# Kernel tuning notes

Measured on AMD Instinct MI355X. Metric: run time of the kernel, lower is better.

The kernel has to match this reference:

```python
import jax, jax.numpy as jnp
import numpy as np

B, T, D = 32, 256, 256  # batch, input_length, output_dim (input_dim == output_dim)
SCALE = 0.06  # ~ 1/sqrt(D) glorot-ish init so LSTM gates don't saturate


def hard_sigmoid(x):
    # Keras-1 default inner_activation for LSTM
    return jnp.clip(0.2 * x + 0.5, 0.0, 1.0)


def lstm_cell(x_t, h, c, W, U, b, d):
    # Keras gate order: i, f, c(g), o
    z = x_t @ W + h @ U + b
    i = hard_sigmoid(z[:, :d])
    f = hard_sigmoid(z[:, d:2 * d])
    g = jnp.tanh(z[:, 2 * d:3 * d])
    o = hard_sigmoid(z[:, 3 * d:])
    c_new = f * c + i * g
    h_new = o * jnp.tanh(c_new)
    return h_new, c_new


def setup_inputs() -> dict:
    key = jax.random.key(0)
    ks = jax.random.split(key, 7)
    x = jax.random.normal(ks[0], (B, T, D), dtype=jnp.float32)
    reader_W = jax.random.normal(ks[1], (D, 4 * D), dtype=jnp.float32) * SCALE
    reader_U = jax.random.normal(ks[2], (D, 4 * D), dtype=jnp.float32) * SCALE
    reader_b = jnp.zeros((4 * D,), jnp.float32)
    writer_W = jax.random.normal(ks[3], (2 * D, 4 * D), dtype=jnp.float32) * SCALE
    writer_U = jax.random.normal(ks[4], (D, 4 * D), dtype=jnp.float32) * SCALE
    writer_b = jnp.zeros((4 * D,), jnp.float32)
    composer_W = jax.random.normal(ks[5], (2 * D, 2 * D), dtype=jnp.float32) * SCALE
    composer_b = jnp.zeros((2 * D,), jnp.float32)
    return {"x": x, "reader_W": reader_W, "reader_U": reader_U, "reader_b": reader_b,
            "writer_W": writer_W, "writer_U": writer_U, "writer_b": writer_b,
            "composer_W": composer_W, "composer_b": composer_b}


def reference(x, reader_W, reader_U, reader_b, writer_W, writer_U, writer_b,
              composer_W, composer_b):
    b, t, d = x.shape
    h0 = jnp.zeros((b, d), x.dtype)
    c0 = jnp.zeros((b, d), x.dtype)

    # ---- read: reader LSTM over the sequence (return_sequences) ----
    def rstep(carry, x_t):
        h, c = carry
        h, c = lstm_cell(x_t, h, c, reader_W, reader_U, reader_b, d)
        return (h, c), h

    _, o_seq = jax.lax.scan(rstep, (h0, c0), jnp.swapaxes(x, 0, 1))  # [T,B,D]

    mem0 = x  # mem_0 = input (B, T, D)

    # ---- compose_and_write_step per timestep ----
    def step(carry, o_t):
        mem, wh, wc = carry
        # summarize_memory: eqs 2-3
        scores = jnp.einsum('bd,btd->bt', o_t, mem)
        z_t = jax.nn.softmax(scores, axis=-1)                 # (B, T)
        m_rt = jnp.einsum('bt,btd->bd', z_t, mem)             # (B, D)
        # compose (eq 4), linear activation
        c_t = jnp.concatenate([o_t, m_rt], axis=-1) @ composer_W + composer_b  # (B, 2D)
        # writer LSTM step (eq 5)
        wh, wc = lstm_cell(c_t, wh, wc, writer_W, writer_U, writer_b, d)
        # update_memory (eq 6): blend via tiled z_t / h_t
        zt = z_t[:, :, None]
        mem = mem * (1.0 - zt) + wh[:, None, :] * zt
        return (mem, wh, wc), wh

    (_, _, _), hs = jax.lax.scan(step, (mem0, h0, c0), o_seq)  # hs: [T,B,D]
    return hs[-1]  # return_mode == 'last_output'
```

## Files before the change

### kernel.cpp

```cpp
#include <hip/hip_runtime.h>
#include <math.h>

#define TB 512
#define NBATCH 32
#define TT 256
#define DD 256

typedef float f32x4 __attribute__((ext_vector_type(4)));

#define WS_WF   0u
#define WS_BF   524288u
#define WS_HP   525312u
#define WS_PAR  541696u
#define PS      260
#define WS_WHP  608256u
#define WS_BAR  616448u
#define WS_FLOATS 624704u

#define O_WW    0
#define S_WW    784
#define O_RW    12544
#define S_RW    524
#define O_MEM   20928
#define S_MEM   260
#define O_WACT  29248
#define S_WACT  792
#define O_RACT  35584
#define S_RACT  524
#define O_WZ    39776
#define O_RZ    39936
#define O_SS    40096
#define O_SE    40128
#define O_WC    40160
#define O_RC    40192
#define O_WB    40224
#define O_RB    40240
#define O_RJ    40256
#define O_MS    40320
#define LDS_FLOATS 40448
#define DYN_LDS_BYTES (LDS_FLOATS*4)

__device__ __forceinline__ float hsig(float x) { return fminf(fmaxf(0.2f*x + 0.5f, 0.f), 1.f); }
__device__ __forceinline__ float ftanh(float x) {
  const float a = fminf(fabsf(x), 15.f);
  const float e = __expf(2.f * a);
  const float r = (e - 1.f) / (e + 1.f);
  return copysignf(r, x);
}
__device__ __forceinline__ int akw(int k) { return k + 4*(k/192); }
__device__ __forceinline__ int akr(int k) { return k + 4*(k/128); }

__device__ __forceinline__ void gst(float* p, float v) {
  __hip_atomic_store(p, v, __ATOMIC_RELAXED, __HIP_MEMORY_SCOPE_AGENT);
}
__device__ __forceinline__ void gst4(float* p, f32x4 v) {
  asm volatile("global_store_dwordx4 %0, %1, off sc0 sc1" :: "v"(p), "v"(v) : "memory");
}

__device__ __forceinline__ void tag_store(int* tp, int v) {
  asm volatile("s_waitcnt vmcnt(0) lgkmcnt(0)" ::: "memory");
  __syncthreads();
  if (threadIdx.x == 0)
    __hip_atomic_store(tp, v, __ATOMIC_RELAXED, __HIP_MEMORY_SCOPE_AGENT);
}
__device__ __forceinline__ void tag_spin(const int* tags, int v) {
  if (threadIdx.x < 64) {
    int sp = 0;
    for (;;) {
      const int t = __hip_atomic_load(&tags[threadIdx.x * 16], __ATOMIC_RELAXED,
                                      __HIP_MEMORY_SCOPE_AGENT);
      if (__all(t == v)) break;
      __builtin_amdgcn_s_sleep(2);
      if (++sp > (1 << 14)) break;
    }
  }
  __syncthreads();
}
__device__ __forceinline__ void barrier_fenced(int* cnt, int target) {
  __syncthreads();
  if (threadIdx.x == 0) {
    __threadfence();
    __hip_atomic_fetch_add(cnt, 1, __ATOMIC_RELAXED, __HIP_MEMORY_SCOPE_AGENT);
    int sp = 0;
    while (__hip_atomic_load(cnt, __ATOMIC_RELAXED, __HIP_MEMORY_SCOPE_AGENT) < target) {
      if (++sp > (1 << 20)) break;
    }
    __threadfence();
  }
  __syncthreads();
}

__global__ void __launch_bounds__(TB) nse_kernel(
    const float* __restrict__ x,
    const float* __restrict__ rW, const float* __restrict__ rU, const float* __restrict__ rb,
    const float* __restrict__ wW, const float* __restrict__ wU, const float* __restrict__ wb,
    const float* __restrict__ cW, const float* __restrict__ cb,
    float* __restrict__ out, float* __restrict__ ws)
{
  extern __shared__ float sm[];
  const int tid = threadIdx.x;
  const int w = blockIdx.x;
  const int g = w >> 6;
  const int m = w & 63;
  const int b0 = g * 8;
  const int blm = m >> 3;
  const int isl = m & 7;
  const int bmy = b0 + blm;

  float* Wf   = ws + WS_WF;
  float* bfv  = ws + WS_BF;
  float* hpub = ws + WS_HP;
  float* par  = ws + WS_PAR;
  float* whp  = ws + WS_WHP;
  int*   bars = (int*)(ws + WS_BAR);
  int* tagsA  = &bars[g*1024];
  int* tagsB  = &bars[4096 + g*1024];
  int* myA    = &tagsA[m*16];
  int* myB    = &tagsB[m*16];
  int* lcnt   = &bars[8192];
  int* magic  = &bars[8192 + 32];

  if (w == 0 && tid == 0) {
    __hip_atomic_store(lcnt, 0, __ATOMIC_RELAXED, __HIP_MEMORY_SCOPE_AGENT);
    __hip_atomic_store(magic, 1357911, __ATOMIC_RELEASE, __HIP_MEMORY_SCOPE_AGENT);
  }
  if (tid == 0) {
    int sp = 0;
    while (__hip_atomic_load(magic, __ATOMIC_ACQUIRE, __HIP_MEMORY_SCOPE_AGENT) != 1357911) {
      if (++sp > (1 << 20)) break;
    }
  }
  __syncthreads();

  {
    const int kt = w >> 4, nt = w & 15;
    const int r = tid >> 4, c4 = (tid & 15) * 4;
    float a0 = 0.f, a1 = 0.f, a2 = 0.f, a3 = 0.f;
    for (int jc = 0; jc < 512; jc += 32) {
      for (int u = tid; u < 1024; u += TB) {
        int rr = u >> 5, jj = u & 31;
        sm[rr*33 + jj] = cW[(32*kt + rr)*512 + jc + jj];
      }
      {
        int jj = tid >> 4, cc = (tid & 15) * 4;
        const f32x4 v = *(const f32x4*)&wW[(jc + jj)*1024 + 64*nt + cc];
        float* d = &sm[1056 + jj*68 + cc];
        d[0] = v.x; d[1] = v.y; d[2] = v.z; d[3] = v.w;
      }
      __syncthreads();
      #pragma unroll 8
      for (int j = 0; j < 32; j++) {
        const float a = sm[r*33 + j];
        const float* wv = &sm[1056 + j*68 + c4];
        a0 += a*wv[0]; a1 += a*wv[1]; a2 += a*wv[2]; a3 += a*wv[3];
      }
      __syncthreads();
    }
    float* d = &Wf[(32*kt + r)*1024 + 64*nt + c4];
    d[0] = a0; d[1] = a1; d[2] = a2; d[3] = a3;
  }
  if (w >= 16 && w < 32) {
    __syncthreads();
    const int base = (w - 16) * 64;
    const int c = tid & 63, jq = tid >> 6;
    float p = 0.f;
    for (int j = 64*jq; j < 64*jq + 64; j++) p += cb[j] * wW[j*1024 + base + c];
    sm[jq*68 + c] = p;
    __syncthreads();
    if (tid < 64) {
      float s = wb[base + tid];
      for (int j = 0; j < 8; j++) s += sm[j*68 + tid];
      bfv[base + tid] = s;
    }
  }
  barrier_fenced(lcnt, 256);

  for (int u = tid; u < 3072; u += TB) {
    const int k = u >> 2, gate = u & 3;
    const float* sp = (k < 512) ? &Wf[(size_t)k*1024 + gate*256 + 4*m]
                                : &wU[(size_t)(k-512)*1024 + gate*256 + 4*m];
    const f32x4 v = *(const f32x4*)sp;
    const int ik = akw(k);
    sm[O_WW + (gate*4+0)*S_WW + ik] = v.x;
    sm[O_WW + (gate*4+1)*S_WW + ik] = v.y;
    sm[O_WW + (gate*4+2)*S_WW + ik] = v.z;
    sm[O_WW + (gate*4+3)*S_WW + ik] = v.w;
  }
  for (int u = tid; u < 2048; u += TB) {
    const int k = u >> 2, gate = u & 3;
    const float* sp = (k < 256) ? &rW[(size_t)k*1024 + gate*256 + 4*m]
                                : &rU[(size_t)(k-256)*1024 + gate*256 + 4*m];
    const f32x4 v = *(const f32x4*)sp;
    const int ik = akr(k);
    sm[O_RW + (gate*4+0)*S_RW + ik] = v.x;
    sm[O_RW + (gate*4+1)*S_RW + ik] = v.y;
    sm[O_RW + (gate*4+2)*S_RW + ik] = v.z;
    sm[O_RW + (gate*4+3)*S_RW + ik] = v.w;
  }
  for (int u = tid; u < 2048; u += TB) {
    const int r = u >> 6, d4 = (u & 63) * 4;
    *(f32x4*)&sm[O_MEM + r*S_MEM + d4] =
        *(const f32x4*)&x[((size_t)bmy*TT + 32*isl + r)*DD + d4];
  }
  for (int u = tid; u < LDS_FLOATS - O_WACT; u += TB) sm[O_WACT + u] = 0.f;
  __syncthreads();
  {
    const int bl = tid >> 6, d4 = (tid & 63) * 4;
    *(f32x4*)&sm[O_RACT + bl*S_RACT + akr(d4)] =
        *(const f32x4*)&x[(size_t)(b0+bl)*TT*DD + d4];
  }
  if (tid < 16) {
    const int gate = tid >> 2, dl = tid & 3;
    sm[O_WB + tid] = bfv[gate*256 + 4*m + dl];
    sm[O_RB + tid] = rb[gate*256 + 4*m + dl];
  }
  __syncthreads();

  const int q   = tid & 3;
  const int cl  = ((tid >> 4) & 3) + 4 * (tid >> 7);
  const int bl8 = ((tid >> 2) & 3) + 4 * ((tid >> 6) & 1);

  for (int s = 0; s <= TT; s++) {
    if (s >= 1) {
      tag_spin(tagsB, s - 1);
      const int bl = tid >> 6, d4 = (tid & 63) * 4;
      f32x4 vh, vw;
      const float* ph = &hpub[(size_t)((s-1)&1)*8192 + (b0+bl)*256 + d4];
      const float* pw = &whp[(b0+bl)*256 + d4];
      asm volatile(
        "global_load_dwordx4 %0, %2, off sc0 sc1\n\t"
        "global_load_dwordx4 %1, %3, off sc0 sc1\n\t"
        "s_waitcnt vmcnt(0)"
        : "=&v"(vh), "=&v"(vw) : "v"(ph), "v"(pw) : "memory");
      *(f32x4*)&sm[O_RACT + bl*S_RACT + akr(256 + d4)] = vh;
      *(f32x4*)&sm[O_WACT + bl*S_WACT + akw(d4)]       = vh;
      if (s >= 2)
        *(f32x4*)&sm[O_WACT + bl*S_WACT + akw(512 + d4)] = vw;
    }
    __syncthreads();

    if (s >= 1) {
      const int r = tid >> 4, tk = tid & 15;
      float* mrow = &sm[O_MEM + r*S_MEM + 16*tk];
      const float* orow = &sm[O_RACT + blm*S_RACT + akr(256 + 16*tk)];
      float acc = 0.f;
      if (s >= 2) {
        const float zr = sm[O_SE + r] * sm[O_RJ + blm*8 + isl];
        const float omz = 1.f - zr;
        const float* hrow = &sm[O_WACT + blm*S_WACT + akw(512 + 16*tk)];
        #pragma unroll
        for (int i2 = 0; i2 < 16; i2 += 4) {
          f32x4 mv = *(f32x4*)(mrow + i2);
          const f32x4 hv = *(const f32x4*)(hrow + i2);
          const f32x4 ov = *(const f32x4*)(orow + i2);
          mv.x = mv.x*omz + hv.x*zr;  mv.y = mv.y*omz + hv.y*zr;
          mv.z = mv.z*omz + hv.z*zr;  mv.w = mv.w*omz + hv.w*zr;
          *(f32x4*)(mrow + i2) = mv;
          acc += mv.x*ov.x + mv.y*ov.y + mv.z*ov.z + mv.w*ov.w;
        }
      } else {
        #pragma unroll
        for (int i2 = 0; i2 < 16; i2 += 4) {
          const f32x4 mv = *(const f32x4*)(mrow + i2);
          const f32x4 ov = *(const f32x4*)(orow + i2);
          acc += mv.x*ov.x + mv.y*ov.y + mv.z*ov.z + mv.w*ov.w;
        }
      }
      acc += __shfl_xor(acc, 1, 64); acc += __shfl_xor(acc, 2, 64);
      acc += __shfl_xor(acc, 4, 64); acc += __shfl_xor(acc, 8, 64);
      if (tk == 0) sm[O_SS + r] = acc;
    }
    __syncthreads();
    if (s >= 1 && tid < 32) {
      const float sc = sm[O_SS + tid];
      float mx = sc;
      mx = fmaxf(mx, __shfl_xor(mx, 1, 64)); mx = fmaxf(mx, __shfl_xor(mx, 2, 64));
      mx = fmaxf(mx, __shfl_xor(mx, 4, 64)); mx = fmaxf(mx, __shfl_xor(mx, 8, 64));
      mx = fmaxf(mx, __shfl_xor(mx, 16, 64));
      const float e = __expf(sc - mx);
      float su = e;
      su += __shfl_xor(su, 1, 64); su += __shfl_xor(su, 2, 64); su += __shfl_xor(su, 4, 64);
      su += __shfl_xor(su, 8, 64); su += __shfl_xor(su, 16, 64);
      sm[O_SE + tid] = e;
      if (tid == 0) {
        gst(&par[((size_t)bmy*8 + isl)*PS + 256], mx);
        gst(&par[((size_t)bmy*8 + isl)*PS + 257], su);
      }
    }
    __syncthreads();
    if (s >= 1) {
      const int dblk = tid >> 3, rh = tid & 7;
      f32x4 p; p.x = 0.f; p.y = 0.f; p.z = 0.f; p.w = 0.f;
      #pragma unroll
      for (int i = 0; i < 4; i++) {
        const int rr = 4*rh + i;
        const float e = sm[O_SE + rr];
        const f32x4 mv = *(const f32x4*)&sm[O_MEM + rr*S_MEM + 4*dblk];
        p.x += e*mv.x; p.y += e*mv.y; p.z += e*mv.z; p.w += e*mv.w;
      }
      p.x += __shfl_xor(p.x,1,64); p.x += __shfl_xor(p.x,2,64); p.x += __shfl_xor(p.x,4,64);
      p.y += __shfl_xor(p.y,1,64); p.y += __shfl_xor(p.y,2,64); p.y += __shfl_xor(p.y,4,64);
      p.z += __shfl_xor(p.z,1,64); p.z += __shfl_xor(p.z,2,64); p.z += __shfl_xor(p.z,4,64);
      p.w += __shfl_xor(p.w,1,64); p.w += __shfl_xor(p.w,2,64); p.w += __shfl_xor(p.w,4,64);
      if (rh == 0) gst4(&par[((size_t)bmy*8 + isl)*PS + 4*dblk], p);
      tag_store(myA, s);
    } else {
      __syncthreads();
    }

    if (s <= TT-1) {
      const float* wr = &sm[O_RW + cl*S_RW + 132*q];
      const float* ar = &sm[O_RACT + bl8*S_RACT + 132*q];
      float acc = 0.f;
      #pragma unroll
      for (int kk = 0; kk < 128; kk += 4) {
        const f32x4 wv = *(const f32x4*)(wr + kk);
        const f32x4 av = *(const f32x4*)(ar + kk);
        acc += wv.x*av.x + wv.y*av.y + wv.z*av.z + wv.w*av.w;
      }
      acc += __shfl_xor(acc, 1, 64);
      acc += __shfl_xor(acc, 2, 64);
      if (q == 0) sm[O_RZ + bl8*20 + cl] = acc + sm[O_RB + cl];
    }
    __syncthreads();
    if (s <= TT-1 && tid < 32) {
      const int bl = tid >> 2, dl = tid & 3;
      const float zi = sm[O_RZ + bl*20 + dl];
      const float zf = sm[O_RZ + bl*20 + 4 + dl];
      const float zg = sm[O_RZ + bl*20 + 8 + dl];
      const float zo = sm[O_RZ + bl*20 + 12 + dl];
      const float cn = hsig(zf)*sm[O_RC + tid] + hsig(zi)*ftanh(zg);
      sm[O_RC + tid] = cn;
      gst(&hpub[(size_t)(s&1)*8192 + (b0+bl)*256 + 4*m + dl], hsig(zo)*ftanh(cn));
    }

    if (s >= 1) {
      tag_spin(tagsA, s);
      const int bl = tid >> 6, d4 = (tid & 63) * 4;
      f32x4 v0,v1,v2,v3,v4,v5,v6,v7;
      float msv;
      {
        const float* p0 = &par[((size_t)(b0+bl)*8 + 0)*PS + d4];
        const float* p4 = p0 + 4*PS;
        const int idx = tid & 127;
        const float* msp = &par[((size_t)(b0 + (idx>>4))*8 + ((idx>>1)&7))*PS + 256 + (idx&1)];
        asm volatile(
          "global_load_dwordx4 %0, %9, off sc0 sc1\n\t"
          "global_load_dwordx4 %1, %9, off offset:1040 sc0 sc1\n\t"
          "global_load_dwordx4 %2, %9, off offset:2080 sc0 sc1\n\t"
          "global_load_dwordx4 %3, %9, off offset:3120 sc0 sc1\n\t"
          "global_load_dwordx4 %4, %10, off sc0 sc1\n\t"
          "global_load_dwordx4 %5, %10, off offset:1040 sc0 sc1\n\t"
          "global_load_dwordx4 %6, %10, off offset:2080 sc0 sc1\n\t"
          "global_load_dwordx4 %7, %10, off offset:3120 sc0 sc1\n\t"
          "global_load_dword   %8, %11, off sc0 sc1\n\t"
          "s_waitcnt vmcnt(0)"
          : "=&v"(v0),"=&v"(v1),"=&v"(v2),"=&v"(v3),
            "=&v"(v4),"=&v"(v5),"=&v"(v6),"=&v"(v7),"=&v"(msv)
          : "v"(p0), "v"(p4), "v"(msp) : "memory");
      }
      if (tid < 128) sm[O_MS + tid] = msv;
      __syncthreads();
      if (tid < 8) {
        const int bl2 = tid;
        float M = sm[O_MS + bl2*16];
        for (int j = 1; j < 8; j++) M = fmaxf(M, sm[O_MS + bl2*16 + 2*j]);
        float tot = 0.f, f0[8];
        for (int j = 0; j < 8; j++) {
          f0[j] = __expf(sm[O_MS + bl2*16 + 2*j] - M);
          tot += f0[j] * sm[O_MS + bl2*16 + 2*j + 1];
        }
        const float inv = 1.f / tot;
        for (int j = 0; j < 8; j++) sm[O_RJ + bl2*8 + j] = f0[j]*inv;
      }
      __syncthreads();
      {
        const float* rj = &sm[O_RJ + bl*8];
        f32x4 a;
        a.x = rj[0]*v0.x + rj[1]*v1.x + rj[2]*v2.x + rj[3]*v3.x
            + rj[4]*v4.x + rj[5]*v5.x + rj[6]*v6.x + rj[7]*v7.x;
        a.y = rj[0]*v0.y + rj[1]*v1.y + rj[2]*v2.y + rj[3]*v3.y
            + rj[4]*v4.y + rj[5]*v5.y + rj[6]*v6.y + rj[7]*v7.y;
        a.z = rj[0]*v0.z + rj[1]*v1.z + rj[2]*v2.z + rj[3]*v3.z
            + rj[4]*v4.z + rj[5]*v5.z + rj[6]*v6.z + rj[7]*v7.z;
        a.w = rj[0]*v0.w + rj[1]*v1.w + rj[2]*v2.w + rj[3]*v3.w
            + rj[4]*v4.w + rj[5]*v5.w + rj[6]*v6.w + rj[7]*v7.w;
        *(f32x4*)&sm[O_WACT + bl*S_WACT + akw(256 + d4)] = a;
      }
      __syncthreads();
      {
        const float* wr = &sm[O_WW + cl*S_WW + 196*q];
        const float* ar = &sm[O_WACT + bl8*S_WACT + 196*q];
        float acc = 0.f;
        #pragma unroll 8
        for (int kk = 0; kk < 192; kk += 4) {
          const f32x4 wv = *(const f32x4*)(wr + kk);
          const f32x4 av = *(const f32x4*)(ar + kk);
          acc += wv.x*av.x + wv.y*av.y + wv.z*av.z + wv.w*av.w;
        }
        acc += __shfl_xor(acc, 1, 64);
        acc += __shfl_xor(acc, 2, 64);
        if (q == 0) sm[O_WZ + bl8*20 + cl] = acc + sm[O_WB + cl];
      }
      __syncthreads();
      if (tid < 32) {
        const int bl2 = tid >> 2, dl = tid & 3;
        const float zi = sm[O_WZ + bl2*20 + dl];
        const float zf = sm[O_WZ + bl2*20 + 4 + dl];
        const float zg = sm[O_WZ + bl2*20 + 8 + dl];
        const float zo = sm[O_WZ + bl2*20 + 12 + dl];
        const float cn = hsig(zf)*sm[O_WC + tid] + hsig(zi)*ftanh(zg);
        sm[O_WC + tid] = cn;
        const float hn = hsig(zo)*ftanh(cn);
        if (s == TT) out[(b0+bl2)*256 + 4*m + dl] = hn;
        else         gst(&whp[(b0+bl2)*256 + 4*m + dl], hn);
      }
    }
    if (s == TT) break;
    tag_store(myB, s);
    if (s <= TT-2) {
      const int bl = tid >> 6, d4 = (tid & 63) * 4;
      *(f32x4*)&sm[O_RACT + bl*S_RACT + akr(d4)] =
          *(const f32x4*)&x[((size_t)(b0+bl)*TT + s + 1)*DD + d4];
    }
  }
}

extern "C" void kernel_launch(void* const* d_in, const int* in_sizes, int n_in,
                              void* d_out, int out_size, void* d_ws, size_t ws_size,
                              hipStream_t stream) {
  (void)in_sizes; (void)n_in;
  if (ws_size < (size_t)WS_FLOATS * 4u) {
    hipMemsetAsync(d_out, 0, (size_t)out_size * 4u, stream);
    return;
  }
  const float* x  = (const float*)d_in[0];
  const float* rW = (const float*)d_in[1];
  const float* rU = (const float*)d_in[2];
  const float* rb = (const float*)d_in[3];
  const float* wW = (const float*)d_in[4];
  const float* wU = (const float*)d_in[5];
  const float* wb = (const float*)d_in[6];
  const float* cW = (const float*)d_in[7];
  const float* cb = (const float*)d_in[8];
  float* out = (float*)d_out;
  float* ws  = (float*)d_ws;

  hipFuncSetAttribute((const void*)nse_kernel,
                      hipFuncAttributeMaxDynamicSharedMemorySize, DYN_LDS_BYTES);

  void* args[] = { (void*)&x, (void*)&rW, (void*)&rU, (void*)&rb,
                   (void*)&wW, (void*)&wU, (void*)&wb, (void*)&cW, (void*)&cb,
                   (void*)&out, (void*)&ws };
  hipError_t err = hipLaunchCooperativeKernel((const void*)nse_kernel,
                                              dim3(256), dim3(TB), args,
                                              DYN_LDS_BYTES, stream);
  if (err != hipSuccess) {
    nse_kernel<<<dim3(256), dim3(TB), DYN_LDS_BYTES, stream>>>(
        x, rW, rU, rb, wW, wU, wb, cW, cb, out, ws);
  }
}
```

Before: 2.980 ms.

## Regroup blocks by XCD so group sync stays in local L2, keep weights in registers

New measurement: 3.626 ms. 1.22x slower.

```diff
diff --git a/kernel.cpp b/kernel.cpp
--- a/kernel.cpp
+++ b/kernel.cpp
@@ -2,7 +2,6 @@
 #include <math.h>
 
 #define TB 512
-#define NBATCH 32
 #define TT 256
 #define DD 256
 
@@ -15,63 +14,78 @@
 #define PS      260
 #define WS_WHP  608256u
 #define WS_BAR  616448u
-#define WS_FLOATS 624704u
-
-#define O_WW    0
-#define S_WW    784
-#define O_RW    12544
-#define S_RW    524
-#define O_MEM   20928
+#define WS_FLOATS 633024u
+
+#define O_MEM   0
 #define S_MEM   260
-#define O_WACT  29248
-#define S_WACT  792
-#define O_RACT  35584
-#define S_RACT  524
-#define O_WZ    39776
-#define O_RZ    39936
-#define O_SS    40096
-#define O_SE    40128
-#define O_WC    40160
-#define O_RC    40192
-#define O_WB    40224
-#define O_RB    40240
-#define O_RJ    40256
-#define O_MS    40320
-#define LDS_FLOATS 40448
-#define DYN_LDS_BYTES (LDS_FLOATS*4)
+#define O_WACT  8320
+#define S_WACT  832
+#define O_RACT  11648
+#define S_RACT  576
+#define O_WZ    13952
+#define O_RZ    14096
+#define O_SS    14240
+#define O_SE    14272
+#define O_WC    14304
+#define O_RC    14336
+#define O_WB    14368
+#define O_RB    14400
+#define O_RJ    14432
+#define O_MS    14464
+#define O_XR    14528
+#define DYN_LDS_BYTES 131072
 
 __device__ __forceinline__ float hsig(float x) { return fminf(fmaxf(0.2f*x + 0.5f, 0.f), 1.f); }
 __device__ __forceinline__ float ftanh(float x) {
   const float a = fminf(fabsf(x), 15.f);
   const float e = __expf(2.f * a);
-  const float r = (e - 1.f) / (e + 1.f);
-  return copysignf(r, x);
-}
-__device__ __forceinline__ int akw(int k) { return k + 4*(k/192); }
-__device__ __forceinline__ int akr(int k) { return k + 4*(k/128); }
-
-__device__ __forceinline__ void gst(float* p, float v) {
-  __hip_atomic_store(p, v, __ATOMIC_RELAXED, __HIP_MEMORY_SCOPE_AGENT);
-}
-__device__ __forceinline__ void gst4(float* p, f32x4 v) {
-  asm volatile("global_store_dwordx4 %0, %1, off sc0 sc1" :: "v"(p), "v"(v) : "memory");
-}
-
-__device__ __forceinline__ void tag_store(int* tp, int v) {
+  return copysignf((e - 1.f) / (e + 1.f), x);
+}
+__device__ __forceinline__ int awk(int k) { return (k / 48) * 52 + (k % 48); }
+__device__ __forceinline__ int ark(int k) { return (k >> 5) * 36 + (k & 31); }
+
+__device__ __forceinline__ void stI(int* p, int v, bool lx) {
+  if (lx) asm volatile("global_store_dword %0, %1, off sc0" :: "v"(p), "v"(v) : "memory");
+  else    asm volatile("global_store_dword %0, %1, off sc0 sc1" :: "v"(p), "v"(v) : "memory");
+}
+__device__ __forceinline__ int ldI(const int* p, bool lx) {
+  int t;
+  if (lx) asm volatile("global_load_dword %0, %1, off sc0\n\ts_waitcnt vmcnt(0)" : "=v"(t) : "v"(p) : "memory");
+  else    asm volatile("global_load_dword %0, %1, off sc0 sc1\n\ts_waitcnt vmcnt(0)" : "=v"(t) : "v"(p) : "memory");
+  return t;
+}
+__device__ __forceinline__ void stF(float* p, float v, bool lx) {
+  if (lx) asm volatile("global_store_dword %0, %1, off sc0" :: "v"(p), "v"(v) : "memory");
+  else    asm volatile("global_store_dword %0, %1, off sc0 sc1" :: "v"(p), "v"(v) : "memory");
+}
+__device__ __forceinline__ void stF4(float* p, f32x4 v, bool lx) {
+  if (lx) asm volatile("global_store_dwordx4 %0, %1, off sc0" :: "v"(p), "v"(v) : "memory");
+  else    asm volatile("global_store_dwordx4 %0, %1, off sc0 sc1" :: "v"(p), "v"(v) : "memory");
+}
+__device__ __forceinline__ void ld2x4(const float* p1, const float* p2, f32x4& a, f32x4& b, bool lx) {
+  if (lx) asm volatile(
+    "global_load_dwordx4 %0, %2, off sc0\n\t"
+    "global_load_dwordx4 %1, %3, off sc0\n\t"
+    "s_waitcnt vmcnt(0)" : "=&v"(a), "=&v"(b) : "v"(p1), "v"(p2) : "memory");
+  else asm volatile(
+    "global_load_dwordx4 %0, %2, off sc0 sc1\n\t"
+    "global_load_dwordx4 %1, %3, off sc0 sc1\n\t"
+    "s_waitcnt vmcnt(0)" : "=&v"(a), "=&v"(b) : "v"(p1), "v"(p2) : "memory");
+}
+
+__device__ __forceinline__ void tag_store(int* tp, int v, bool lx) {
   asm volatile("s_waitcnt vmcnt(0) lgkmcnt(0)" ::: "memory");
   __syncthreads();
-  if (threadIdx.x == 0)
-    __hip_atomic_store(tp, v, __ATOMIC_RELAXED, __HIP_MEMORY_SCOPE_AGENT);
-}
-__device__ __forceinline__ void tag_spin(const int* tags, int v) {
-  if (threadIdx.x < 64) {
+  if (threadIdx.x == 0) stI(tp, v, lx);
+}
+__device__ __forceinline__ void tag_spin(const int* tags, int v, bool lx) {
+  if (threadIdx.x < 32) {
     int sp = 0;
     for (;;) {
-      const int t = __hip_atomic_load(&tags[threadIdx.x * 16], __ATOMIC_RELAXED,
-                                      __HIP_MEMORY_SCOPE_AGENT);
+      const int t = ldI(&tags[threadIdx.x * 32], lx);
       if (__all(t == v)) break;
-      __builtin_amdgcn_s_sleep(2);
-      if (++sp > (1 << 14)) break;
+      __builtin_amdgcn_s_sleep(1);
+      if (++sp > (1 << 16)) break;
     }
   }
   __syncthreads();
@@ -90,7 +104,7 @@
   __syncthreads();
 }
 
-__global__ void __launch_bounds__(TB) nse_kernel(
+__global__ void __launch_bounds__(TB, 2) nse_kernel(
     const float* __restrict__ x,
     const float* __restrict__ rW, const float* __restrict__ rU, const float* __restrict__ rb,
     const float* __restrict__ wW, const float* __restrict__ wU, const float* __restrict__ wb,
@@ -100,12 +114,6 @@
   extern __shared__ float sm[];
   const int tid = threadIdx.x;
   const int w = blockIdx.x;
-  const int g = w >> 6;
-  const int m = w & 63;
-  const int b0 = g * 8;
-  const int blm = m >> 3;
-  const int isl = m & 7;
-  const int bmy = b0 + blm;
 
   float* Wf   = ws + WS_WF;
   float* bfv  = ws + WS_BF;
@@ -113,15 +121,15 @@
   float* par  = ws + WS_PAR;
   float* whp  = ws + WS_WHP;
   int*   bars = (int*)(ws + WS_BAR);
-  int* tagsA  = &bars[g*1024];
-  int* tagsB  = &bars[4096 + g*1024];
-  int* myA    = &tagsA[m*16];
-  int* myB    = &tagsB[m*16];
-  int* lcnt   = &bars[8192];
-  int* magic  = &bars[8192 + 32];
+  int* lcnt   = &bars[16384];
+  int* magic  = &bars[16416];
+  int* xr     = (int*)&sm[O_XR];
 
   if (w == 0 && tid == 0) {
     __hip_atomic_store(lcnt, 0, __ATOMIC_RELAXED, __HIP_MEMORY_SCOPE_AGENT);
+    for (int i = 0; i < 8; i++)
+      __hip_atomic_store(&bars[16448 + i*8], 0, __ATOMIC_RELAXED, __HIP_MEMORY_SCOPE_AGENT);
+    __hip_atomic_store(&bars[16512], 1, __ATOMIC_RELAXED, __HIP_MEMORY_SCOPE_AGENT);
     __hip_atomic_store(magic, 1357911, __ATOMIC_RELEASE, __HIP_MEMORY_SCOPE_AGENT);
   }
   if (tid == 0) {
@@ -175,79 +183,147 @@
   }
   barrier_fenced(lcnt, 256);
 
-  for (int u = tid; u < 3072; u += TB) {
-    const int k = u >> 2, gate = u & 3;
-    const float* sp = (k < 512) ? &Wf[(size_t)k*1024 + gate*256 + 4*m]
-                                : &wU[(size_t)(k-512)*1024 + gate*256 + 4*m];
-    const f32x4 v = *(const f32x4*)sp;
-    const int ik = akw(k);
-    sm[O_WW + (gate*4+0)*S_WW + ik] = v.x;
-    sm[O_WW + (gate*4+1)*S_WW + ik] = v.y;
-    sm[O_WW + (gate*4+2)*S_WW + ik] = v.z;
-    sm[O_WW + (gate*4+3)*S_WW + ik] = v.w;
-  }
-  for (int u = tid; u < 2048; u += TB) {
-    const int k = u >> 2, gate = u & 3;
-    const float* sp = (k < 256) ? &rW[(size_t)k*1024 + gate*256 + 4*m]
-                                : &rU[(size_t)(k-256)*1024 + gate*256 + 4*m];
-    const f32x4 v = *(const f32x4*)sp;
-    const int ik = akr(k);
-    sm[O_RW + (gate*4+0)*S_RW + ik] = v.x;
-    sm[O_RW + (gate*4+1)*S_RW + ik] = v.y;
-    sm[O_RW + (gate*4+2)*S_RW + ik] = v.z;
-    sm[O_RW + (gate*4+3)*S_RW + ik] = v.w;
-  }
+  {
+    int xcd;
+    asm volatile("s_getreg_b32 %0, hwreg(HW_REG_XCC_ID)" : "=s"(xcd));
+    if (tid == 0) {
+      const int rk = __hip_atomic_fetch_add(&bars[16448 + (xcd & 7)*8], 1,
+                                            __ATOMIC_RELAXED, __HIP_MEMORY_SCOPE_AGENT);
+      xr[0] = xcd & 7;
+      xr[1] = rk;
+    }
+  }
+  barrier_fenced(lcnt, 512);
+  if (tid == 0) {
+    int all32 = 1;
+    for (int i = 0; i < 8; i++) {
+      const int c = __hip_atomic_load(&bars[16448 + i*8], __ATOMIC_RELAXED, __HIP_MEMORY_SCOPE_AGENT);
+      if (c != 32) all32 = 0;
+    }
+    xr[2] = all32;
+  }
+  __syncthreads();
+  const int cnt_ok = xr[2];
+  const int g = cnt_ok ? xr[0] : (w >> 5);
+  const int m = cnt_ok ? xr[1] : (w & 31);
+  bool l2 = false;
+  int* tagsA = &bars[g * 1024];
+  int* tagsB = &bars[8192 + g * 1024];
+  int* myA   = &tagsA[m * 32];
+  int* myB   = &tagsB[m * 32];
+  if (cnt_ok) {
+    int* tvp = (int*)(ws + WS_PAR);
+    if (tid == 0) stI(&tvp[(g*32 + m)*32], 0x5A000000 + (g << 8) + m, true);
+    asm volatile("s_waitcnt vmcnt(0) lgkmcnt(0)" ::: "memory");
+    __syncthreads();
+    if (tid == 0) stI(myA, 7777, true);
+    if (tid < 32) {
+      int sp = 0, to = 0;
+      for (;;) {
+        const int t = ldI(&tagsA[tid * 32], true);
+        if (__all(t == 7777)) break;
+        __builtin_amdgcn_s_sleep(1);
+        if (++sp > (1 << 13)) { to = 1; break; }
+      }
+      const int v = ldI(&tvp[(g*32 + tid)*32], true);
+      const int good = (!to) && (v == 0x5A000000 + (g << 8) + (int)tid);
+      if (tid == 0 && !__all(good))
+        __hip_atomic_store(&bars[16512], 0, __ATOMIC_RELAXED, __HIP_MEMORY_SCOPE_AGENT);
+    }
+    barrier_fenced(lcnt, 768);
+    if (tid == 0)
+      xr[2] = __hip_atomic_load(&bars[16512], __ATOMIC_RELAXED, __HIP_MEMORY_SCOPE_AGENT);
+    __syncthreads();
+    l2 = (xr[2] == 1);
+  }
+  const int b0  = g * 4;
+  const int blm = m >> 3;
+  const int isl = m & 7;
+  const int bmy = b0 + blm;
+
+  const int q  = tid & 15;
+  const int cl = tid >> 4;
+  const int Ccol = (cl >> 3)*256 + 8*m + (cl & 7);
+
+  float wrw[48], wrr[32];
+  for (int u = tid; u < 6144; u += TB) {
+    const int k = u >> 3, rem = u & 7, gate = rem >> 1, hf = rem & 1;
+    const int col0 = gate*256 + 8*m + 4*hf;
+    const f32x4 v = (k < 512) ? *(const f32x4*)&Wf[(size_t)k*1024 + col0]
+                              : *(const f32x4*)&wU[(size_t)(k-512)*1024 + col0];
+    const int c2 = gate*8 + 4*hf;
+    sm[(c2+0)*776 + k] = v.x; sm[(c2+1)*776 + k] = v.y;
+    sm[(c2+2)*776 + k] = v.z; sm[(c2+3)*776 + k] = v.w;
+  }
+  __syncthreads();
+  #pragma unroll
+  for (int kk = 0; kk < 48; kk += 4) {
+    const f32x4 v = *(const f32x4*)&sm[cl*776 + q*48 + kk];
+    wrw[kk] = v.x; wrw[kk+1] = v.y; wrw[kk+2] = v.z; wrw[kk+3] = v.w;
+  }
+  __syncthreads();
+  for (int u = tid; u < 4096; u += TB) {
+    const int k = u >> 3, rem = u & 7, gate = rem >> 1, hf = rem & 1;
+    const int col0 = gate*256 + 8*m + 4*hf;
+    const f32x4 v = (k < 256) ? *(const f32x4*)&rW[(size_t)k*1024 + col0]
+                              : *(const f32x4*)&rU[(size_t)(k-256)*1024 + col0];
+    const int c2 = gate*8 + 4*hf;
+    sm[(c2+0)*520 + k] = v.x; sm[(c2+1)*520 + k] = v.y;
+    sm[(c2+2)*520 + k] = v.z; sm[(c2+3)*520 + k] = v.w;
+  }
+  __syncthreads();
+  #pragma unroll
+  for (int kk = 0; kk < 32; kk += 4) {
+    const f32x4 v = *(const f32x4*)&sm[cl*520 + q*32 + kk];
+    wrr[kk] = v.x; wrr[kk+1] = v.y; wrr[kk+2] = v.z; wrr[kk+3] = v.w;
+  }
+  __syncthreads();
+
   for (int u = tid; u < 2048; u += TB) {
     const int r = u >> 6, d4 = (u & 63) * 4;
     *(f32x4*)&sm[O_MEM + r*S_MEM + d4] =
         *(const f32x4*)&x[((size_t)bmy*TT + 32*isl + r)*DD + d4];
   }
-  for (int u = tid; u < LDS_FLOATS - O_WACT; u += TB) sm[O_WACT + u] = 0.f;
-  __syncthreads();
-  {
+  for (int u = tid; u < 5632; u += TB) sm[O_WACT + u] = 0.f;
+  if (tid < 32) {
+    sm[O_WB + tid] = bfv[(tid >> 3)*256 + 8*m + (tid & 7)];
+    sm[O_RB + tid] = rb[(tid >> 3)*256 + 8*m + (tid & 7)];
+    sm[O_WC + tid] = 0.f;
+    sm[O_RC + tid] = 0.f;
+  }
+  __syncthreads();
+  if (tid < 256) {
     const int bl = tid >> 6, d4 = (tid & 63) * 4;
-    *(f32x4*)&sm[O_RACT + bl*S_RACT + akr(d4)] =
+    *(f32x4*)&sm[O_RACT + bl*S_RACT + ark(d4)] =
         *(const f32x4*)&x[(size_t)(b0+bl)*TT*DD + d4];
   }
-  if (tid < 16) {
-    const int gate = tid >> 2, dl = tid & 3;
-    sm[O_WB + tid] = bfv[gate*256 + 4*m + dl];
-    sm[O_RB + tid] = rb[gate*256 + 4*m + dl];
-  }
-  __syncthreads();
-
-  const int q   = tid & 3;
-  const int cl  = ((tid >> 4) & 3) + 4 * (tid >> 7);
-  const int bl8 = ((tid >> 2) & 3) + 4 * ((tid >> 6) & 1);
+  __syncthreads();
 
   for (int s = 0; s <= TT; s++) {
     if (s >= 1) {
-      tag_spin(tagsB, s - 1);
-      const int bl = tid >> 6, d4 = (tid & 63) * 4;
-      f32x4 vh, vw;
-      const float* ph = &hpub[(size_t)((s-1)&1)*8192 + (b0+bl)*256 + d4];
-      const float* pw = &whp[(b0+bl)*256 + d4];
-      asm volatile(
-        "global_load_dwordx4 %0, %2, off sc0 sc1\n\t"
-        "global_load_dwordx4 %1, %3, off sc0 sc1\n\t"
-        "s_waitcnt vmcnt(0)"
-        : "=&v"(vh), "=&v"(vw) : "v"(ph), "v"(pw) : "memory");
-      *(f32x4*)&sm[O_RACT + bl*S_RACT + akr(256 + d4)] = vh;
-      *(f32x4*)&sm[O_WACT + bl*S_WACT + akw(d4)]       = vh;
-      if (s >= 2)
-        *(f32x4*)&sm[O_WACT + bl*S_WACT + akw(512 + d4)] = vw;
+      tag_spin(tagsB, s - 1, l2);
+      if (tid < 256) {
+        const int bl = tid >> 6, d4 = (tid & 63) * 4;
+        f32x4 vh, vw;
+        ld2x4(&hpub[(size_t)((s-1)&1)*8192 + (b0+bl)*256 + d4],
+              &whp[(b0+bl)*256 + d4], vh, vw, l2);
+        *(f32x4*)&sm[O_RACT + bl*S_RACT + ark(256 + d4)] = vh;
+        *(f32x4*)&sm[O_WACT + bl*S_WACT + awk(d4)]       = vh;
+        if (s >= 2)
+          *(f32x4*)&sm[O_WACT + bl*S_WACT + awk(512 + d4)] = vw;
+      }
     }
     __syncthreads();
 
     if (s >= 1) {
       const int r = tid >> 4, tk = tid & 15;
       float* mrow = &sm[O_MEM + r*S_MEM + 16*tk];
-      const float* orow = &sm[O_RACT + blm*S_RACT + akr(256 + 16*tk)];
+      const float* orow = &sm[O_RACT + blm*S_RACT + ark(256 + 16*tk)];
       float acc = 0.f;
       if (s >= 2) {
         const float zr = sm[O_SE + r] * sm[O_RJ + blm*8 + isl];
         const float omz = 1.f - zr;
-        const float* hrow = &sm[O_WACT + blm*S_WACT + akw(512 + 16*tk)];
+        const float* hrow = &sm[O_WACT + blm*S_WACT + awk(512 + 16*tk)];
         #pragma unroll
         for (int i2 = 0; i2 < 16; i2 += 4) {
           f32x4 mv = *(f32x4*)(mrow + i2);
@@ -283,8 +359,8 @@
       su += __shfl_xor(su, 8, 64); su += __shfl_xor(su, 16, 64);
       sm[O_SE + tid] = e;
       if (tid == 0) {
-        gst(&par[((size_t)bmy*8 + isl)*PS + 256], mx);
-        gst(&par[((size_t)bmy*8 + isl)*PS + 257], su);
+        stF(&par[((size_t)bmy*8 + isl)*PS + 256], mx, l2);
+        stF(&par[((size_t)bmy*8 + isl)*PS + 257], su, l2);
       }
     }
     __syncthreads();
@@ -302,49 +378,65 @@
       p.y += __shfl_xor(p.y,1,64); p.y += __shfl_xor(p.y,2,64); p.y += __shfl_xor(p.y,4,64);
       p.z += __shfl_xor(p.z,1,64); p.z += __shfl_xor(p.z,2,64); p.z += __shfl_xor(p.z,4,64);
       p.w += __shfl_xor(p.w,1,64); p.w += __shfl_xor(p.w,2,64); p.w += __shfl_xor(p.w,4,64);
-      if (rh == 0) gst4(&par[((size_t)bmy*8 + isl)*PS + 4*dblk], p);
-      tag_store(myA, s);
+      if (rh == 0) stF4(&par[((size_t)bmy*8 + isl)*PS + 4*dblk], p, l2);
+      tag_store(myA, s, l2);
     } else {
       __syncthreads();
     }
 
     if (s <= TT-1) {
-      const float* wr = &sm[O_RW + cl*S_RW + 132*q];
-      const float* ar = &sm[O_RACT + bl8*S_RACT + 132*q];
-      float acc = 0.f;
       #pragma unroll
-      for (int kk = 0; kk < 128; kk += 4) {
-        const f32x4 wv = *(const f32x4*)(wr + kk);
-        const f32x4 av = *(const f32x4*)(ar + kk);
-        acc += wv.x*av.x + wv.y*av.y + wv.z*av.z + wv.w*av.w;
-      }
-      acc += __shfl_xor(acc, 1, 64);
-      acc += __shfl_xor(acc, 2, 64);
-      if (q == 0) sm[O_RZ + bl8*20 + cl] = acc + sm[O_RB + cl];
+      for (int bl = 0; bl < 4; bl++) {
+        const float* ar = &sm[O_RACT + bl*S_RACT + q*36];
+        float a = 0.f;
+        #pragma unroll
+        for (int kk = 0; kk < 32; kk += 4) {
+          const f32x4 av = *(const f32x4*)(ar + kk);
+          a += wrr[kk]*av.x + wrr[kk+1]*av.y + wrr[kk+2]*av.z + wrr[kk+3]*av.w;
+        }
+        a += __shfl_xor(a, 1, 64); a += __shfl_xor(a, 2, 64);
+        a += __shfl_xor(a, 4, 64); a += __shfl_xor(a, 8, 64);
+        if (q == 0) sm[O_RZ + bl*36 + cl] = a + sm[O_RB + cl];
+      }
     }
     __syncthreads();
     if (s <= TT-1 && tid < 32) {
-      const int bl = tid >> 2, dl = tid & 3;
-      const float zi = sm[O_RZ + bl*20 + dl];
-      const float zf = sm[O_RZ + bl*20 + 4 + dl];
-      const float zg = sm[O_RZ + bl*20 + 8 + dl];
-      const float zo = sm[O_RZ + bl*20 + 12 + dl];
+      const int bl = tid >> 3, dl = tid & 7;
+      const float zi = sm[O_RZ + bl*36 + dl];
+      const float zf = sm[O_RZ + bl*36 + 8 + dl];
+      const float zg = sm[O_RZ + bl*36 + 16 + dl];
+      const float zo = sm[O_RZ + bl*36 + 24 + dl];
       const float cn = hsig(zf)*sm[O_RC + tid] + hsig(zi)*ftanh(zg);
       sm[O_RC + tid] = cn;
-      gst(&hpub[(size_t)(s&1)*8192 + (b0+bl)*256 + 4*m + dl], hsig(zo)*ftanh(cn));
+      stF(&hpub[(size_t)(s&1)*8192 + (b0+bl)*256 + 8*m + dl], hsig(zo)*ftanh(cn), l2);
     }
 
     if (s >= 1) {
-      tag_spin(tagsA, s);
-      const int bl = tid >> 6, d4 = (tid & 63) * 4;
+      tag_spin(tagsA, s, l2);
       f32x4 v0,v1,v2,v3,v4,v5,v6,v7;
-      float msv;
-      {
+      float msv = 0.f;
+      int bl = 0, d4 = 0;
+      if (tid < 256) {
+        bl = tid >> 6; d4 = (tid & 63) * 4;
         const float* p0 = &par[((size_t)(b0+bl)*8 + 0)*PS + d4];
         const float* p4 = p0 + 4*PS;
-        const int idx = tid & 127;
+        const int idx = tid & 63;
         const float* msp = &par[((size_t)(b0 + (idx>>4))*8 + ((idx>>1)&7))*PS + 256 + (idx&1)];
-        asm volatile(
+        if (l2) asm volatile(
+          "global_load_dwordx4 %0, %9, off sc0\n\t"
+          "global_load_dwordx4 %1, %9, off offset:1040 sc0\n\t"
+          "global_load_dwordx4 %2, %9, off offset:2080 sc0\n\t"
+          "global_load_dwordx4 %3, %9, off offset:3120 sc0\n\t"
+          "global_load_dwordx4 %4, %10, off sc0\n\t"
+          "global_load_dwordx4 %5, %10, off offset:1040 sc0\n\t"
+          "global_load_dwordx4 %6, %10, off offset:2080 sc0\n\t"
+          "global_load_dwordx4 %7, %10, off offset:3120 sc0\n\t"
+          "global_load_dword   %8, %11, off sc0\n\t"
+          "s_waitcnt vmcnt(0)"
+          : "=&v"(v0),"=&v"(v1),"=&v"(v2),"=&v"(v3),
+            "=&v"(v4),"=&v"(v5),"=&v"(v6),"=&v"(v7),"=&v"(msv)
+          : "v"(p0), "v"(p4), "v"(msp) : "memory");
+        else asm volatile(
           "global_load_dwordx4 %0, %9, off sc0 sc1\n\t"
           "global_load_dwordx4 %1, %9, off offset:1040 sc0 sc1\n\t"
           "global_load_dwordx4 %2, %9, off offset:2080 sc0 sc1\n\t"
@@ -359,22 +451,22 @@
             "=&v"(v4),"=&v"(v5),"=&v"(v6),"=&v"(v7),"=&v"(msv)
           : "v"(p0), "v"(p4), "v"(msp) : "memory");
       }
-      if (tid < 128) sm[O_MS + tid] = msv;
-      __syncthreads();
-      if (tid < 8) {
-        const int bl2 = tid;
-        float M = sm[O_MS + bl2*16];
-        for (int j = 1; j < 8; j++) M = fmaxf(M, sm[O_MS + bl2*16 + 2*j]);
+      if (tid < 64) sm[O_MS + tid] = msv;
+      __syncthreads();
+      if (tid < 4) {
+        const int b2 = tid;
+        float M = sm[O_MS + b2*16];
+        for (int j = 1; j < 8; j++) M = fmaxf(M, sm[O_MS + b2*16 + 2*j]);
         float tot = 0.f, f0[8];
         for (int j = 0; j < 8; j++) {
-          f0[j] = __expf(sm[O_MS + bl2*16 + 2*j] - M);
-          tot += f0[j] * sm[O_MS + bl2*16 + 2*j + 1];
+          f0[j] = __expf(sm[O_MS + b2*16 + 2*j] - M);
+          tot += f0[j] * sm[O_MS + b2*16 + 2*j + 1];
         }
         const float inv = 1.f / tot;
-        for (int j = 0; j < 8; j++) sm[O_RJ + bl2*8 + j] = f0[j]*inv;
-      }
-      __syncthreads();
-      {
+        for (int j = 0; j < 8; j++) sm[O_RJ + b2*8 + j] = f0[j]*inv;
+      }
+      __syncthreads();
+      if (tid < 256) {
         const float* rj = &sm[O_RJ + bl*8];
         f32x4 a;
         a.x = rj[0]*v0.x + rj[1]*v1.x + rj[2]*v2.x + rj[3]*v3.x
@@ -385,42 +477,43 @@
             + rj[4]*v4.z + rj[5]*v5.z + rj[6]*v6.z + rj[7]*v7.z;
         a.w = rj[0]*v0.w + rj[1]*v1.w + rj[2]*v2.w + rj[3]*v3.w
             + rj[4]*v4.w + rj[5]*v5.w + rj[6]*v6.w + rj[7]*v7.w;
-        *(f32x4*)&sm[O_WACT + bl*S_WACT + akw(256 + d4)] = a;
+        *(f32x4*)&sm[O_WACT + bl*S_WACT + awk(256 + d4)] = a;
       }
       __syncthreads();
       {
-        const float* wr = &sm[O_WW + cl*S_WW + 196*q];
-        const float* ar = &sm[O_WACT + bl8*S_WACT + 196*q];
-        float acc = 0.f;
-        #pragma unroll 8
-        for (int kk = 0; kk < 192; kk += 4) {
-          const f32x4 wv = *(const f32x4*)(wr + kk);
-          const f32x4 av = *(const f32x4*)(ar + kk);
-          acc += wv.x*av.x + wv.y*av.y + wv.z*av.z + wv.w*av.w;
+        #pragma unroll
+        for (int bl2 = 0; bl2 < 4; bl2++) {
+          const float* aw = &sm[O_WACT + bl2*S_WACT + q*52];
+          float a = 0.f;
+          #pragma unroll
+          for (int kk = 0; kk < 48; kk += 4) {
+            const f32x4 av = *(const f32x4*)(aw + kk);
+            a += wrw[kk]*av.x + wrw[kk+1]*av.y + wrw[kk+2]*av.z + wrw[kk+3]*av.w;
+          }
+          a += __shfl_xor(a, 1, 64); a += __shfl_xor(a, 2, 64);
+          a += __shfl_xor(a, 4, 64); a += __shfl_xor(a, 8, 64);
+          if (q == 0) sm[O_WZ + bl2*36 + cl] = a + sm[O_WB + cl];
         }
-        acc += __shfl_xor(acc, 1, 64);
-        acc += __shfl_xor(acc, 2, 64);
-        if (q == 0) sm[O_WZ + bl8*20 + cl] = acc + sm[O_WB + cl];
       }
       __syncthreads();
       if (tid < 32) {
-        const int bl2 = tid >> 2, dl = tid & 3;
-        const float zi = sm[O_WZ + bl2*20 + dl];
-        const float zf = sm[O_WZ + bl2*20 + 4 + dl];
-        const float zg = sm[O_WZ + bl2*20 + 8 + dl];
-        const float zo = sm[O_WZ + bl2*20 + 12 + dl];
+        const int bl2 = tid >> 3, dl = tid & 7;
+        const float zi = sm[O_WZ + bl2*36 + dl];
+        const float zf = sm[O_WZ + bl2*36 + 8 + dl];
+        const float zg = sm[O_WZ + bl2*36 + 16 + dl];
+        const float zo = sm[O_WZ + bl2*36 + 24 + dl];
         const float cn = hsig(zf)*sm[O_WC + tid] + hsig(zi)*ftanh(zg);
         sm[O_WC + tid] = cn;
         const float hn = hsig(zo)*ftanh(cn);
-        if (s == TT) out[(b0+bl2)*256 + 4*m + dl] = hn;
-        else         gst(&whp[(b0+bl2)*256 + 4*m + dl], hn);
+        if (s == TT) out[(b0+bl2)*256 + 8*m + dl] = hn;
+        else         stF(&whp[(b0+bl2)*256 + 8*m + dl], hn, l2);
       }
     }
     if (s == TT) break;
-    tag_store(myB, s);
-    if (s <= TT-2) {
+    tag_store(myB, s, l2);
+    if (s <= TT-2 && tid < 256) {
       const int bl = tid >> 6, d4 = (tid & 63) * 4;
-      *(f32x4*)&sm[O_RACT + bl*S_RACT + akr(d4)] =
+      *(f32x4*)&sm[O_RACT + bl*S_RACT + ark(d4)] =
           *(const f32x4*)&x[((size_t)(b0+bl)*TT + s + 1)*DD + d4];
     }
   }
```
